# Performance work log

Hardware: AMD Instinct MI355X
Metric: run time of the kernel (lower is better)

## Reference

```python
import jax, jax.numpy as jnp
import numpy as np

N_USER, N_ITEM, N_REL = 200000, 100000, 64
DIM = 64
S_UU = S_UI = S_IU = S_II = 8
BATCH = 65536
MAX_RATING = 5.0


def setup_inputs() -> dict:
    key = jax.random.key(0)
    ks = jax.random.split(key, 24)
    inp = {}
    # query batch
    inp['u'] = jax.random.randint(ks[0], (BATCH,), 0, N_USER)
    inp['v'] = jax.random.randint(ks[1], (BATCH,), 0, N_ITEM)
    # embedding tables (init std=0.8 as in the torch code)
    inp['usr_feat'] = 0.8 * jax.random.normal(ks[2], (N_USER, DIM), jnp.float32)
    inp['item_feat'] = 0.8 * jax.random.normal(ks[3], (N_ITEM, DIM), jnp.float32)
    inp['rel_feat'] = 0.8 * jax.random.normal(ks[4], (N_REL, DIM), jnp.float32)
    # precomputed sampled neighbor tables (built once in __init__ in the original)
    inp['neigh_uu'] = jax.random.randint(ks[5], (N_USER, S_UU), 0, N_USER)
    inp['neigh_uu_st'] = jax.random.uniform(ks[6], (N_USER, S_UU), jnp.float32)
    inp['neigh_ui'] = jax.random.randint(ks[7], (N_USER, S_UI), 0, N_ITEM)
    inp['neigh_ui_rat'] = MAX_RATING * jax.random.uniform(ks[8], (N_USER, S_UI), jnp.float32)
    inp['neigh_ui_vot'] = jax.random.uniform(ks[9], (N_USER, S_UI), jnp.float32)
    inp['neigh_ui_tim'] = jax.random.uniform(ks[10], (N_USER, S_UI), jnp.float32)
    inp['neigh_iu'] = jax.random.randint(ks[11], (N_ITEM, S_IU), 0, N_USER)
    inp['neigh_iu_rat'] = MAX_RATING * jax.random.uniform(ks[12], (N_ITEM, S_IU), jnp.float32)
    inp['neigh_iu_vot'] = jax.random.uniform(ks[13], (N_ITEM, S_IU), jnp.float32)
    inp['neigh_iu_tim'] = jax.random.uniform(ks[14], (N_ITEM, S_IU), jnp.float32)
    inp['neigh_ii'] = jax.random.randint(ks[15], (N_ITEM, S_II), 0, N_ITEM)
    inp['neigh_ir'] = jax.random.randint(ks[16], (N_ITEM, S_II), 0, N_REL)
    # aggregator transforms (one per side)
    sc = 1.0 / np.sqrt(DIM)
    inp['Wu'] = sc * jax.random.normal(ks[17], (DIM, DIM), jnp.float32)
    inp['bu'] = jnp.zeros((DIM,), jnp.float32)
    inp['Wv'] = sc * jax.random.normal(ks[18], (DIM, DIM), jnp.float32)
    inp['bv'] = jnp.zeros((DIM,), jnp.float32)
    return inp


def reference(u, v, usr_feat, item_feat, rel_feat,
              neigh_uu, neigh_uu_st, neigh_ui, neigh_ui_rat, neigh_ui_vot, neigh_ui_tim,
              neigh_iu, neigh_iu_rat, neigh_iu_vot, neigh_iu_tim, neigh_ii, neigh_ir,
              Wu, bu, Wv, bv):
    u_emb = usr_feat[u]                                   # [B, D]
    v_emb = item_feat[v]                                  # [B, D]

    # ---- user-side aggregation ----
    # social neighbors, weighted by softmax over social tie strength
    uu_nei = usr_feat[neigh_uu[u]]                        # [B, S, D]
    w_uu = jax.nn.softmax(neigh_uu_st[u], axis=-1)        # [B, S]
    agg_uu = jnp.einsum('bs,bsd->bd', w_uu, uu_nei)
    # interacted items, weighted by rating * vote * time recency
    ui_nei = item_feat[neigh_ui[u]]                       # [B, S, D]
    s_ui = neigh_ui_rat[u] * neigh_ui_vot[u] * neigh_ui_tim[u]
    w_ui = jax.nn.softmax(s_ui, axis=-1)
    agg_ui = jnp.einsum('bs,bsd->bd', w_ui, ui_nei)
    user_h = jax.nn.relu((u_emb + agg_uu + agg_ui) @ Wu + bu)

    # ---- item-side aggregation ----
    # users who interacted with the item, weighted like above
    iu_nei = usr_feat[neigh_iu[v]]                        # [B, S, D]
    s_iu = neigh_iu_rat[v] * neigh_iu_vot[v] * neigh_iu_tim[v]
    w_iu = jax.nn.softmax(s_iu, axis=-1)
    agg_iu = jnp.einsum('bs,bsd->bd', w_iu, iu_nei)
    # KG neighbors with user-relation attention (KGCN-style)
    ii_nei = item_feat[neigh_ii[v]]                       # [B, S, D]
    rel = rel_feat[neigh_ir[v]]                           # [B, S, D]
    att = jnp.einsum('bd,bsd->bs', u_emb, rel)            # user-relation score
    w_ii = jax.nn.softmax(att, axis=-1)
    agg_ii = jnp.einsum('bs,bsd->bd', w_ii, ii_nei)
    item_h = jax.nn.relu((v_emb + agg_iu + agg_ii) @ Wv + bv)

    # rating prediction
    score = jax.nn.sigmoid(jnp.sum(user_h * item_h, axis=-1)) * MAX_RATING
    return score
```

## Files before the change

### kernel.cpp

```cpp
#include <hip/hip_runtime.h>
#include <math.h>

constexpr int DIM = 64;
constexpr int S = 8;
constexpr int WPB = 8;
constexpr int BLOCK = WPB * 64;
constexpr int WSTR = 68;

__global__ __launch_bounds__(BLOCK)
void sestkgcn_kernel(
    const int*   __restrict__ u_idx,
    const int*   __restrict__ v_idx,
    const float* __restrict__ usr_feat,
    const float* __restrict__ item_feat,
    const float* __restrict__ rel_feat,
    const int*   __restrict__ neigh_uu,
    const float* __restrict__ neigh_uu_st,
    const int*   __restrict__ neigh_ui,
    const float* __restrict__ neigh_ui_rat,
    const float* __restrict__ neigh_ui_vot,
    const float* __restrict__ neigh_ui_tim,
    const int*   __restrict__ neigh_iu,
    const float* __restrict__ neigh_iu_rat,
    const float* __restrict__ neigh_iu_vot,
    const float* __restrict__ neigh_iu_tim,
    const int*   __restrict__ neigh_ii,
    const int*   __restrict__ neigh_ir,
    const float* __restrict__ Wu,
    const float* __restrict__ bu,
    const float* __restrict__ Wv,
    const float* __restrict__ bv,
    float*       __restrict__ out,
    int n)
{
    __shared__ float sWuT[DIM * WSTR];
    __shared__ float sWvT[DIM * WSTR];
    __shared__ float sbu[DIM];
    __shared__ float sbv[DIM];
    __shared__ float xs[WPB * DIM];

    const int tid = threadIdx.x;
    for (int i = tid; i < DIM * DIM; i += BLOCK) {
        const int d_ = i >> 6, j_ = i & 63;
        sWuT[j_ * WSTR + d_] = Wu[i];
        sWvT[j_ * WSTR + d_] = Wv[i];
    }
    if (tid < DIM) { sbu[tid] = bu[tid]; sbv[tid] = bv[tid]; }
    __syncthreads();

    const int wave = tid >> 6;
    const int lane = tid & 63;
    const int b = blockIdx.x * WPB + wave;
    if (b >= n) return;

    const int u = u_idx[b];
    const int v = v_idx[b];

    const float u_d = usr_feat[(long)u * DIM + lane];
    const float v_d = item_feat[(long)v * DIM + lane];

    float* xw = &xs[wave * DIM];
    const float4* wuT = (const float4*)&sWuT[lane * WSTR];
    const float4* wvT = (const float4*)&sWvT[lane * WSTR];
    const float4* xw4 = (const float4*)xw;

    float w[S];
    {
        float m = -INFINITY;
        #pragma unroll
        for (int s = 0; s < S; s++) { w[s] = neigh_uu_st[(long)u * S + s]; m = fmaxf(m, w[s]); }
        float sum = 0.f;
        #pragma unroll
        for (int s = 0; s < S; s++) { w[s] = __expf(w[s] - m); sum += w[s]; }
        float inv = 1.0f / sum;
        #pragma unroll
        for (int s = 0; s < S; s++) w[s] *= inv;
    }
    float agg_uu = 0.f;
    {
        int ni[S];
        #pragma unroll
        for (int s = 0; s < S; s++) ni[s] = neigh_uu[(long)u * S + s];
        float r[S];
        #pragma unroll
        for (int s = 0; s < S; s++) r[s] = usr_feat[(long)ni[s] * DIM + lane];
        #pragma unroll
        for (int s = 0; s < S; s++) agg_uu = fmaf(w[s], r[s], agg_uu);
    }

    {
        float m = -INFINITY;
        #pragma unroll
        for (int s = 0; s < S; s++) {
            float sc = neigh_ui_rat[(long)u * S + s] * neigh_ui_vot[(long)u * S + s]
                     * neigh_ui_tim[(long)u * S + s];
            w[s] = sc; m = fmaxf(m, sc);
        }
        float sum = 0.f;
        #pragma unroll
        for (int s = 0; s < S; s++) { w[s] = __expf(w[s] - m); sum += w[s]; }
        float inv = 1.0f / sum;
        #pragma unroll
        for (int s = 0; s < S; s++) w[s] *= inv;
    }
    float agg_ui = 0.f;
    {
        int ni[S];
        #pragma unroll
        for (int s = 0; s < S; s++) ni[s] = neigh_ui[(long)u * S + s];
        float r[S];
        #pragma unroll
        for (int s = 0; s < S; s++) r[s] = item_feat[(long)ni[s] * DIM + lane];
        #pragma unroll
        for (int s = 0; s < S; s++) agg_ui = fmaf(w[s], r[s], agg_ui);
    }

    float hu;
    {
        xw[lane] = u_d + agg_uu + agg_ui;
        __threadfence_block();
        float a0 = 0.f, a1 = 0.f, a2 = 0.f, a3 = 0.f;
        #pragma unroll
        for (int k = 0; k < DIM / 4; k++) {
            float4 xv = xw4[k];
            float4 wv = wuT[k];
            a0 = fmaf(xv.x, wv.x, a0);
            a1 = fmaf(xv.y, wv.y, a1);
            a2 = fmaf(xv.z, wv.z, a2);
            a3 = fmaf(xv.w, wv.w, a3);
        }
        hu = fmaxf((a0 + a1) + (a2 + a3) + sbu[lane], 0.f);
    }

    {
        float m = -INFINITY;
        #pragma unroll
        for (int s = 0; s < S; s++) {
            float sc = neigh_iu_rat[(long)v * S + s] * neigh_iu_vot[(long)v * S + s]
                     * neigh_iu_tim[(long)v * S + s];
            w[s] = sc; m = fmaxf(m, sc);
        }
        float sum = 0.f;
        #pragma unroll
        for (int s = 0; s < S; s++) { w[s] = __expf(w[s] - m); sum += w[s]; }
        float inv = 1.0f / sum;
        #pragma unroll
        for (int s = 0; s < S; s++) w[s] *= inv;
    }
    float agg_iu = 0.f;
    {
        int ni[S];
        #pragma unroll
        for (int s = 0; s < S; s++) ni[s] = neigh_iu[(long)v * S + s];
        float r[S];
        #pragma unroll
        for (int s = 0; s < S; s++) r[s] = usr_feat[(long)ni[s] * DIM + lane];
        #pragma unroll
        for (int s = 0; s < S; s++) agg_iu = fmaf(w[s], r[s], agg_iu);
    }

    {
        int nr[S];
        #pragma unroll
        for (int s = 0; s < S; s++) nr[s] = neigh_ir[(long)v * S + s];
        #pragma unroll
        for (int s = 0; s < S; s++) {
            float p = u_d * rel_feat[(long)nr[s] * DIM + lane];
            #pragma unroll
            for (int off = 32; off > 0; off >>= 1) p += __shfl_xor(p, off);
            w[s] = p;
        }
        float m = -INFINITY;
        #pragma unroll
        for (int s = 0; s < S; s++) m = fmaxf(m, w[s]);
        float sum = 0.f;
        #pragma unroll
        for (int s = 0; s < S; s++) { w[s] = __expf(w[s] - m); sum += w[s]; }
        float inv = 1.0f / sum;
        #pragma unroll
        for (int s = 0; s < S; s++) w[s] *= inv;
    }
    float agg_ii = 0.f;
    {
        int ni[S];
        #pragma unroll
        for (int s = 0; s < S; s++) ni[s] = neigh_ii[(long)v * S + s];
        float r[S];
        #pragma unroll
        for (int s = 0; s < S; s++) r[s] = item_feat[(long)ni[s] * DIM + lane];
        #pragma unroll
        for (int s = 0; s < S; s++) agg_ii = fmaf(w[s], r[s], agg_ii);
    }

    float hv;
    {
        xw[lane] = v_d + agg_iu + agg_ii;
        __threadfence_block();
        float a0 = 0.f, a1 = 0.f, a2 = 0.f, a3 = 0.f;
        #pragma unroll
        for (int k = 0; k < DIM / 4; k++) {
            float4 xv = xw4[k];
            float4 wv = wvT[k];
            a0 = fmaf(xv.x, wv.x, a0);
            a1 = fmaf(xv.y, wv.y, a1);
            a2 = fmaf(xv.z, wv.z, a2);
            a3 = fmaf(xv.w, wv.w, a3);
        }
        hv = fmaxf((a0 + a1) + (a2 + a3) + sbv[lane], 0.f);
    }

    float p = hu * hv;
    #pragma unroll
    for (int off = 32; off > 0; off >>= 1) p += __shfl_xor(p, off);
    if (lane == 0) out[b] = 5.0f / (1.0f + __expf(-p));
}

extern "C" void kernel_launch(void* const* d_in, const int* in_sizes, int n_in,
                              void* d_out, int out_size, void* d_ws, size_t ws_size,
                              hipStream_t stream) {
    const int*   u_idx        = (const int*)  d_in[0];
    const int*   v_idx        = (const int*)  d_in[1];
    const float* usr_feat     = (const float*)d_in[2];
    const float* item_feat    = (const float*)d_in[3];
    const float* rel_feat     = (const float*)d_in[4];
    const int*   neigh_uu     = (const int*)  d_in[5];
    const float* neigh_uu_st  = (const float*)d_in[6];
    const int*   neigh_ui     = (const int*)  d_in[7];
    const float* neigh_ui_rat = (const float*)d_in[8];
    const float* neigh_ui_vot = (const float*)d_in[9];
    const float* neigh_ui_tim = (const float*)d_in[10];
    const int*   neigh_iu     = (const int*)  d_in[11];
    const float* neigh_iu_rat = (const float*)d_in[12];
    const float* neigh_iu_vot = (const float*)d_in[13];
    const float* neigh_iu_tim = (const float*)d_in[14];
    const int*   neigh_ii     = (const int*)  d_in[15];
    const int*   neigh_ir     = (const int*)  d_in[16];
    const float* Wu           = (const float*)d_in[17];
    const float* bu           = (const float*)d_in[18];
    const float* Wv           = (const float*)d_in[19];
    const float* bv           = (const float*)d_in[20];
    float*       out          = (float*)d_out;

    const int n = in_sizes[0];
    const int blocks = (n + WPB - 1) / WPB;
    sestkgcn_kernel<<<blocks, BLOCK, 0, stream>>>(
        u_idx, v_idx, usr_feat, item_feat, rel_feat,
        neigh_uu, neigh_uu_st, neigh_ui, neigh_ui_rat, neigh_ui_vot, neigh_ui_tim,
        neigh_iu, neigh_iu_rat, neigh_iu_vot, neigh_iu_tim, neigh_ii, neigh_ir,
        Wu, bu, Wv, bv, out, n);
}
```

Before: 292.2 us.

## Use persistent grid-stride loop with lane-parallel softmax and transposed attention reduction

Switches to a persistent grid of 1024 blocks that grid-stride over the batch, so the transposed weight matrices are staged into shared memory once per block rather than once per 8 samples. Softmax scores are now loaded one per lane in groups of 8 and reduced with shuffles instead of every lane redundantly loading all 8. Neighbor indices are read as int4 vectors, and the 8 relation-attention dot products share one transposed shuffle tree instead of 8 full butterflies. Index math uses 32-bit unsigned arithmetic, and the fixed grid may reduce the latency-hiding occupancy available to this gather-bound kernel.

Result: faster. 254.6 us (-12.9%).

```diff
diff --git a/kernel.cpp b/kernel.cpp
--- a/kernel.cpp
+++ b/kernel.cpp
@@ -5,7 +5,23 @@
 constexpr int S = 8;
 constexpr int WPB = 8;
 constexpr int BLOCK = WPB * 64;
+constexpr int GRID = 1024;
 constexpr int WSTR = 68;
+
+__device__ __forceinline__ void octet_softmax(float sc, float* wout) {
+    float m = sc;
+    m = fmaxf(m, __shfl_xor(m, 1));
+    m = fmaxf(m, __shfl_xor(m, 2));
+    m = fmaxf(m, __shfl_xor(m, 4));
+    float e = __expf(sc - m);
+    float s = e;
+    s += __shfl_xor(s, 1);
+    s += __shfl_xor(s, 2);
+    s += __shfl_xor(s, 4);
+    float w = e / s;
+    #pragma unroll
+    for (int k = 0; k < 8; k++) wout[k] = __shfl(w, k);
+}
 
 __global__ __launch_bounds__(BLOCK)
 void sestkgcn_kernel(
@@ -50,169 +66,150 @@
 
     const int wave = tid >> 6;
     const int lane = tid & 63;
-    const int b = blockIdx.x * WPB + wave;
-    if (b >= n) return;
-
-    const int u = u_idx[b];
-    const int v = v_idx[b];
-
-    const float u_d = usr_feat[(long)u * DIM + lane];
-    const float v_d = item_feat[(long)v * DIM + lane];
+    const int ls   = lane & 7;
 
     float* xw = &xs[wave * DIM];
     const float4* wuT = (const float4*)&sWuT[lane * WSTR];
     const float4* wvT = (const float4*)&sWvT[lane * WSTR];
     const float4* xw4 = (const float4*)xw;
-
-    float w[S];
-    {
-        float m = -INFINITY;
+    const float bu_l = sbu[lane];
+    const float bv_l = sbv[lane];
+
+    const int stride = GRID * WPB;
+    for (int b = blockIdx.x * WPB + wave; b < n; b += stride) {
+        const int u = u_idx[b];
+        const int v = v_idx[b];
+        const unsigned u8 = (unsigned)u << 3, v8 = (unsigned)v << 3;
+        const unsigned u64o = (unsigned)u << 6, v64o = (unsigned)v << 6;
+
+        const float u_d = usr_feat[u64o | (unsigned)lane];
+        const float v_d = item_feat[v64o | (unsigned)lane];
+
+        const float sc_uu = neigh_uu_st[u8 + ls];
+        const float sc_ui = neigh_ui_rat[u8 + ls] * neigh_ui_vot[u8 + ls] * neigh_ui_tim[u8 + ls];
+        const float sc_iu = neigh_iu_rat[v8 + ls] * neigh_iu_vot[v8 + ls] * neigh_iu_tim[v8 + ls];
+
+        float w[S];
+        octet_softmax(sc_uu, w);
+        float agg_uu = 0.f;
+        {
+            const int4 i0 = ((const int4*)(neigh_uu + u8))[0];
+            const int4 i1 = ((const int4*)(neigh_uu + u8))[1];
+            const int ni[S] = {i0.x, i0.y, i0.z, i0.w, i1.x, i1.y, i1.z, i1.w};
+            float r[S];
+            #pragma unroll
+            for (int s = 0; s < S; s++) r[s] = usr_feat[((unsigned)ni[s] << 6) | (unsigned)lane];
+            #pragma unroll
+            for (int s = 0; s < S; s++) agg_uu = fmaf(w[s], r[s], agg_uu);
+        }
+
+        octet_softmax(sc_ui, w);
+        float agg_ui = 0.f;
+        {
+            const int4 i0 = ((const int4*)(neigh_ui + u8))[0];
+            const int4 i1 = ((const int4*)(neigh_ui + u8))[1];
+            const int ni[S] = {i0.x, i0.y, i0.z, i0.w, i1.x, i1.y, i1.z, i1.w};
+            float r[S];
+            #pragma unroll
+            for (int s = 0; s < S; s++) r[s] = item_feat[((unsigned)ni[s] << 6) | (unsigned)lane];
+            #pragma unroll
+            for (int s = 0; s < S; s++) agg_ui = fmaf(w[s], r[s], agg_ui);
+        }
+
+        float hu;
+        {
+            xw[lane] = u_d + agg_uu + agg_ui;
+            __threadfence_block();
+            float a0 = 0.f, a1 = 0.f, a2 = 0.f, a3 = 0.f;
+            #pragma unroll
+            for (int k = 0; k < DIM / 4; k++) {
+                float4 xv = xw4[k];
+                float4 wv = wuT[k];
+                a0 = fmaf(xv.x, wv.x, a0);
+                a1 = fmaf(xv.y, wv.y, a1);
+                a2 = fmaf(xv.z, wv.z, a2);
+                a3 = fmaf(xv.w, wv.w, a3);
+            }
+            hu = fmaxf((a0 + a1) + (a2 + a3) + bu_l, 0.f);
+        }
+
+        octet_softmax(sc_iu, w);
+        float agg_iu = 0.f;
+        {
+            const int4 i0 = ((const int4*)(neigh_iu + v8))[0];
+            const int4 i1 = ((const int4*)(neigh_iu + v8))[1];
+            const int ni[S] = {i0.x, i0.y, i0.z, i0.w, i1.x, i1.y, i1.z, i1.w};
+            float r[S];
+            #pragma unroll
+            for (int s = 0; s < S; s++) r[s] = usr_feat[((unsigned)ni[s] << 6) | (unsigned)lane];
+            #pragma unroll
+            for (int s = 0; s < S; s++) agg_iu = fmaf(w[s], r[s], agg_iu);
+        }
+
+        {
+            const int4 r0 = ((const int4*)(neigh_ir + v8))[0];
+            const int4 r1 = ((const int4*)(neigh_ir + v8))[1];
+            const int nr[S] = {r0.x, r0.y, r0.z, r0.w, r1.x, r1.y, r1.z, r1.w};
+            float p[S];
+            #pragma unroll
+            for (int s = 0; s < S; s++) p[s] = u_d * rel_feat[((unsigned)nr[s] << 6) | (unsigned)lane];
+
+            float m1[4];
+            #pragma unroll
+            for (int i = 0; i < 4; i++) {
+                float lo = (lane & 1) ? p[2 * i + 1] : p[2 * i];
+                float hi = (lane & 1) ? p[2 * i]     : p[2 * i + 1];
+                m1[i] = lo + __shfl_xor(hi, 1);
+            }
+            float m2[2];
+            #pragma unroll
+            for (int i = 0; i < 2; i++) {
+                float lo = (lane & 2) ? m1[2 * i + 1] : m1[2 * i];
+                float hi = (lane & 2) ? m1[2 * i]     : m1[2 * i + 1];
+                m2[i] = lo + __shfl_xor(hi, 2);
+            }
+            float lo = (lane & 4) ? m2[1] : m2[0];
+            float hi = (lane & 4) ? m2[0] : m2[1];
+            float att = lo + __shfl_xor(hi, 4);
+            att += __shfl_xor(att, 8);
+            att += __shfl_xor(att, 16);
+            att += __shfl_xor(att, 32);
+            octet_softmax(att, w);
+        }
+        float agg_ii = 0.f;
+        {
+            const int4 i0 = ((const int4*)(neigh_ii + v8))[0];
+            const int4 i1 = ((const int4*)(neigh_ii + v8))[1];
+            const int ni[S] = {i0.x, i0.y, i0.z, i0.w, i1.x, i1.y, i1.z, i1.w};
+            float r[S];
+            #pragma unroll
+            for (int s = 0; s < S; s++) r[s] = item_feat[((unsigned)ni[s] << 6) | (unsigned)lane];
+            #pragma unroll
+            for (int s = 0; s < S; s++) agg_ii = fmaf(w[s], r[s], agg_ii);
+        }
+
+        float hv;
+        {
+            xw[lane] = v_d + agg_iu + agg_ii;
+            __threadfence_block();
+            float a0 = 0.f, a1 = 0.f, a2 = 0.f, a3 = 0.f;
+            #pragma unroll
+            for (int k = 0; k < DIM / 4; k++) {
+                float4 xv = xw4[k];
+                float4 wv = wvT[k];
+                a0 = fmaf(xv.x, wv.x, a0);
+                a1 = fmaf(xv.y, wv.y, a1);
+                a2 = fmaf(xv.z, wv.z, a2);
+                a3 = fmaf(xv.w, wv.w, a3);
+            }
+            hv = fmaxf((a0 + a1) + (a2 + a3) + bv_l, 0.f);
+        }
+
+        float p = hu * hv;
         #pragma unroll
-        for (int s = 0; s < S; s++) { w[s] = neigh_uu_st[(long)u * S + s]; m = fmaxf(m, w[s]); }
-        float sum = 0.f;
-        #pragma unroll
-        for (int s = 0; s < S; s++) { w[s] = __expf(w[s] - m); sum += w[s]; }
-        float inv = 1.0f / sum;
-        #pragma unroll
-        for (int s = 0; s < S; s++) w[s] *= inv;
+        for (int off = 32; off > 0; off >>= 1) p += __shfl_xor(p, off);
+        if (lane == 0) out[b] = 5.0f / (1.0f + __expf(-p));
     }
-    float agg_uu = 0.f;
-    {
-        int ni[S];
-        #pragma unroll
-        for (int s = 0; s < S; s++) ni[s] = neigh_uu[(long)u * S + s];
-        float r[S];
-        #pragma unroll
-        for (int s = 0; s < S; s++) r[s] = usr_feat[(long)ni[s] * DIM + lane];
-        #pragma unroll
-        for (int s = 0; s < S; s++) agg_uu = fmaf(w[s], r[s], agg_uu);
-    }
-
-    {
-        float m = -INFINITY;
-        #pragma unroll
-        for (int s = 0; s < S; s++) {
-            float sc = neigh_ui_rat[(long)u * S + s] * neigh_ui_vot[(long)u * S + s]
-                     * neigh_ui_tim[(long)u * S + s];
-            w[s] = sc; m = fmaxf(m, sc);
-        }
-        float sum = 0.f;
-        #pragma unroll
-        for (int s = 0; s < S; s++) { w[s] = __expf(w[s] - m); sum += w[s]; }
-        float inv = 1.0f / sum;
-        #pragma unroll
-        for (int s = 0; s < S; s++) w[s] *= inv;
-    }
-    float agg_ui = 0.f;
-    {
-        int ni[S];
-        #pragma unroll
-        for (int s = 0; s < S; s++) ni[s] = neigh_ui[(long)u * S + s];
-        float r[S];
-        #pragma unroll
-        for (int s = 0; s < S; s++) r[s] = item_feat[(long)ni[s] * DIM + lane];
-        #pragma unroll
-        for (int s = 0; s < S; s++) agg_ui = fmaf(w[s], r[s], agg_ui);
-    }
-
-    float hu;
-    {
-        xw[lane] = u_d + agg_uu + agg_ui;
-        __threadfence_block();
-        float a0 = 0.f, a1 = 0.f, a2 = 0.f, a3 = 0.f;
-        #pragma unroll
-        for (int k = 0; k < DIM / 4; k++) {
-            float4 xv = xw4[k];
-            float4 wv = wuT[k];
-            a0 = fmaf(xv.x, wv.x, a0);
-            a1 = fmaf(xv.y, wv.y, a1);
-            a2 = fmaf(xv.z, wv.z, a2);
-            a3 = fmaf(xv.w, wv.w, a3);
-        }
-        hu = fmaxf((a0 + a1) + (a2 + a3) + sbu[lane], 0.f);
-    }
-
-    {
-        float m = -INFINITY;
-        #pragma unroll
-        for (int s = 0; s < S; s++) {
-            float sc = neigh_iu_rat[(long)v * S + s] * neigh_iu_vot[(long)v * S + s]
-                     * neigh_iu_tim[(long)v * S + s];
-            w[s] = sc; m = fmaxf(m, sc);
-        }
-        float sum = 0.f;
-        #pragma unroll
-        for (int s = 0; s < S; s++) { w[s] = __expf(w[s] - m); sum += w[s]; }
-        float inv = 1.0f / sum;
-        #pragma unroll
-        for (int s = 0; s < S; s++) w[s] *= inv;
-    }
-    float agg_iu = 0.f;
-    {
-        int ni[S];
-        #pragma unroll
-        for (int s = 0; s < S; s++) ni[s] = neigh_iu[(long)v * S + s];
-        float r[S];
-        #pragma unroll
-        for (int s = 0; s < S; s++) r[s] = usr_feat[(long)ni[s] * DIM + lane];
-        #pragma unroll
-        for (int s = 0; s < S; s++) agg_iu = fmaf(w[s], r[s], agg_iu);
-    }
-
-    {
-        int nr[S];
-        #pragma unroll
-        for (int s = 0; s < S; s++) nr[s] = neigh_ir[(long)v * S + s];
-        #pragma unroll
-        for (int s = 0; s < S; s++) {
-            float p = u_d * rel_feat[(long)nr[s] * DIM + lane];
-            #pragma unroll
-            for (int off = 32; off > 0; off >>= 1) p += __shfl_xor(p, off);
-            w[s] = p;
-        }
-        float m = -INFINITY;
-        #pragma unroll
-        for (int s = 0; s < S; s++) m = fmaxf(m, w[s]);
-        float sum = 0.f;
-        #pragma unroll
-        for (int s = 0; s < S; s++) { w[s] = __expf(w[s] - m); sum += w[s]; }
-        float inv = 1.0f / sum;
-        #pragma unroll
-        for (int s = 0; s < S; s++) w[s] *= inv;
-    }
-    float agg_ii = 0.f;
-    {
-        int ni[S];
-        #pragma unroll
-        for (int s = 0; s < S; s++) ni[s] = neigh_ii[(long)v * S + s];
-        float r[S];
-        #pragma unroll
-        for (int s = 0; s < S; s++) r[s] = item_feat[(long)ni[s] * DIM + lane];
-        #pragma unroll
-        for (int s = 0; s < S; s++) agg_ii = fmaf(w[s], r[s], agg_ii);
-    }
-
-    float hv;
-    {
-        xw[lane] = v_d + agg_iu + agg_ii;
-        __threadfence_block();
-        float a0 = 0.f, a1 = 0.f, a2 = 0.f, a3 = 0.f;
-        #pragma unroll
-        for (int k = 0; k < DIM / 4; k++) {
-            float4 xv = xw4[k];
-            float4 wv = wvT[k];
-            a0 = fmaf(xv.x, wv.x, a0);
-            a1 = fmaf(xv.y, wv.y, a1);
-            a2 = fmaf(xv.z, wv.z, a2);
-            a3 = fmaf(xv.w, wv.w, a3);
-        }
-        hv = fmaxf((a0 + a1) + (a2 + a3) + sbv[lane], 0.f);
-    }
-
-    float p = hu * hv;
-    #pragma unroll
-    for (int off = 32; off > 0; off >>= 1) p += __shfl_xor(p, off);
-    if (lane == 0) out[b] = 5.0f / (1.0f + __expf(-p));
 }
 
 extern "C" void kernel_launch(void* const* d_in, const int* in_sizes, int n_in,
@@ -242,7 +239,8 @@
     float*       out          = (float*)d_out;
 
     const int n = in_sizes[0];
-    const int blocks = (n + WPB - 1) / WPB;
+    int blocks = (n + WPB - 1) / WPB;
+    if (blocks > GRID) blocks = GRID;
     sestkgcn_kernel<<<blocks, BLOCK, 0, stream>>>(
         u_idx, v_idx, usr_feat, item_feat, rel_feat,
         neigh_uu, neigh_uu_st, neigh_ui, neigh_ui_rat, neigh_ui_vot, neigh_ui_tim,
```
